# Performance work log

Measured on AMD Instinct MI355X. Metric: run time of the kernel, lower is better.

Reference implementation:

```python
import jax, jax.numpy as jnp
import numpy as np
from jax import lax

B, W_LEN, V, E, C, K, L = 8, 1000, 50000, 100, 50, 3, 18000


def setup_inputs() -> dict:
    key = jax.random.key(0)
    ks = jax.random.split(key, 7)
    return {
        "x": jax.random.randint(ks[0], (B, W_LEN), 0, V),
        "W_embed": jax.random.normal(ks[1], (V, E), dtype=jnp.float32) * 0.1,
        "conv_w": jax.random.normal(ks[2], (C, E, K), dtype=jnp.float32) * 0.08,
        "conv_b": jax.random.normal(ks[3], (C,), dtype=jnp.float32) * 0.01,
        "u_w": jax.random.normal(ks[4], (L, C), dtype=jnp.float32) * 0.1,
        "out_w": jax.random.normal(ks[5], (L, C), dtype=jnp.float32) * 0.1,
        "out_b": jax.random.normal(ks[6], (L,), dtype=jnp.float32) * 0.01,
    }


def reference(x, W_embed, conv_w, conv_b, u_w, out_w, out_b):
    # embedding lookup: (B, W, E)
    emb = W_embed[x]
    # conv1d over sequence, 'same' padding: (B, C, W)
    emb_ncw = jnp.transpose(emb, (0, 2, 1))
    H = lax.conv_general_dilated(
        emb_ncw, conv_w, window_strides=(1,), padding=[(K // 2, K // 2)],
        dimension_numbers=("NCH", "OIH", "NCH"))
    H = jnp.tanh(H + conv_b[None, :, None])
    H = jnp.transpose(H, (0, 2, 1))  # (B, W, C)
    # label-wise attention scores: (B, L, W), softmax over seq
    scores = jnp.einsum("lc,bwc->blw", u_w, H)
    attns = jax.nn.softmax(scores, axis=2)
    # attention-pooled reps: (B, L, C)
    m = jnp.einsum("blw,bwc->blc", attns, H)
    # per-label weighted dot product + bias, sigmoid: (B, L)
    out = jax.nn.sigmoid(jnp.sum(out_w[None] * m, axis=2) + out_b[None])
    return out
```

## Files before the change

kernel.cpp:

```cpp
#include <hip/hip_runtime.h>
#include <hip/hip_bf16.h>
#include <cmath>

#define AS1 __attribute__((address_space(1)))
#define AS3 __attribute__((address_space(3)))

#define B_ 8
#define W_LEN_ 1000
#define WP 1024
#define E_ 100
#define C_ 50
#define CPAD 64
#define HP 72
#define K_ 3
#define L_ 18000
#define TL 64
#define NLBLK ((L_ + TL - 1) / TL)
#define CWT 16
#define NSLOT (K_ * (E_ / 4))

typedef __attribute__((ext_vector_type(8))) short bf16x8;
typedef __attribute__((ext_vector_type(4))) short bf16x4;
typedef __attribute__((ext_vector_type(4))) float f32x4;

static __device__ __forceinline__ void gl_lds16(const void* g, void* l) {
    __builtin_amdgcn_global_load_lds((const AS1 unsigned*)g, (AS3 unsigned*)l, 16, 0, 0);
}
static __device__ __forceinline__ float bf2f(short s) {
    return __uint_as_float(((unsigned)(unsigned short)s) << 16);
}

__global__ __launch_bounds__(256) void prep_w(
    const float* __restrict__ conv_w, bf16x4* __restrict__ cwTs)
{
    int idx = blockIdx.x * blockDim.x + threadIdx.x;
    if (idx >= NSLOT * C_) return;
    int slot = idx / C_;
    int c    = idx % C_;
    int k = slot / (E_ / 4);
    int i = slot % (E_ / 4);
    bf16x4 v;
    #pragma unroll
    for (int q = 0; q < 4; q++) {
        __hip_bfloat16 h = __float2bfloat16(conv_w[((size_t)c * E_ + 4 * i + q) * K_ + k]);
        v[q] = *reinterpret_cast<short*>(&h);
    }
    cwTs[idx] = v;
}

__global__ __launch_bounds__(256) void prep_uo(
    const float* __restrict__ u_w, const float* __restrict__ out_w,
    __hip_bfloat16* __restrict__ UO)
{
    int tid = blockIdx.x * blockDim.x + threadIdx.x;
    if (tid >= 2 * L_ * CPAD) return;
    int c = tid & (CPAD - 1);
    int l = (tid >> 6) % L_;
    int m = tid / (L_ * CPAD);
    const float* src = m ? out_w : u_w;
    float v = (c < C_) ? src[(size_t)l * C_ + c] : 0.f;
    UO[tid] = __float2bfloat16(v);
}

__global__ __launch_bounds__(256) void conv_kernel(
    const int* __restrict__ x,
    const float* __restrict__ W_embed,
    const bf16x4* __restrict__ cwTs,
    const float* __restrict__ conv_b,
    __hip_bfloat16* __restrict__ H)
{
    __shared__ float4 emb_s[(CWT + 2) * (E_ / 4)];
    __shared__ bf16x4 wS[NSLOT * C_];

    const int b  = blockIdx.y;
    const int w0 = blockIdx.x * CWT;
    const int tid = threadIdx.x;

    for (int i = tid; i < NSLOT * C_; i += 256) wS[i] = cwTs[i];

    for (int i = tid; i < (CWT + 2) * (E_ / 4); i += 256) {
        int row = i / (E_ / 4);
        int e4  = i % (E_ / 4);
        int ws  = w0 - 1 + row;
        float4 v = make_float4(0.f, 0.f, 0.f, 0.f);
        if ((unsigned)ws < (unsigned)W_LEN_)
            v = ((const float4*)(W_embed + (size_t)x[b * W_LEN_ + ws] * E_))[e4];
        emb_s[i] = v;
    }
    __syncthreads();

    const int c  = tid & 63;
    const int wq = tid >> 6;
    const int cc = (c < C_) ? c : 0;

    f32x4 acc[4];
    const float bias = conv_b[cc];
    #pragma unroll
    for (int j = 0; j < 4; j++) acc[j] = (f32x4){bias, 0.f, 0.f, 0.f};

    const float4* eb = &emb_s[wq * 4 * (E_ / 4)];

    #pragma unroll 5
    for (int i = 0; i < E_ / 4; i++) {
        bf16x4 kb0 = wS[i * C_ + cc];
        bf16x4 kb1 = wS[(25 + i) * C_ + cc];
        bf16x4 kb2 = wS[(50 + i) * C_ + cc];
        float4 k0 = make_float4(bf2f(kb0[0]), bf2f(kb0[1]), bf2f(kb0[2]), bf2f(kb0[3]));
        float4 k1 = make_float4(bf2f(kb1[0]), bf2f(kb1[1]), bf2f(kb1[2]), bf2f(kb1[3]));
        float4 k2 = make_float4(bf2f(kb2[0]), bf2f(kb2[1]), bf2f(kb2[2]), bf2f(kb2[3]));
        float4 e0 = eb[i],       e1 = eb[25 + i],  e2 = eb[50 + i];
        float4 e3 = eb[75 + i],  e4 = eb[100 + i], e5 = eb[125 + i];
        acc[0].x += e0.x*k0.x + e1.x*k1.x + e2.x*k2.x;
        acc[0].y += e0.y*k0.y + e1.y*k1.y + e2.y*k2.y;
        acc[0].z += e0.z*k0.z + e1.z*k1.z + e2.z*k2.z;
        acc[0].w += e0.w*k0.w + e1.w*k1.w + e2.w*k2.w;
        acc[1].x += e1.x*k0.x + e2.x*k1.x + e3.x*k2.x;
        acc[1].y += e1.y*k0.y + e2.y*k1.y + e3.y*k2.y;
        acc[1].z += e1.z*k0.z + e2.z*k1.z + e3.z*k2.z;
        acc[1].w += e1.w*k0.w + e2.w*k1.w + e3.w*k2.w;
        acc[2].x += e2.x*k0.x + e3.x*k1.x + e4.x*k2.x;
        acc[2].y += e2.y*k0.y + e3.y*k1.y + e4.y*k2.y;
        acc[2].z += e2.z*k0.z + e3.z*k1.z + e4.z*k2.z;
        acc[2].w += e2.w*k0.w + e3.w*k1.w + e4.w*k2.w;
        acc[3].x += e3.x*k0.x + e4.x*k1.x + e5.x*k2.x;
        acc[3].y += e3.y*k0.y + e4.y*k1.y + e5.y*k2.y;
        acc[3].z += e3.z*k0.z + e4.z*k1.z + e5.z*k2.z;
        acc[3].w += e3.w*k0.w + e4.w*k1.w + e5.w*k2.w;
    }

    #pragma unroll
    for (int j = 0; j < 4; j++) {
        int w = w0 + wq * 4 + j;
        float v = 0.f;
        if (c < C_ && w < W_LEN_)
            v = tanhf((acc[j].x + acc[j].z) + (acc[j].y + acc[j].w));
        __hip_bfloat16* row = H + ((size_t)b * WP + w) * HP;
        row[c] = __float2bfloat16(v);
        if (c < HP - 64) row[64 + c] = __float2bfloat16(0.f);
    }
}

__global__ __launch_bounds__(256) void attn_kernel(
    const __hip_bfloat16* __restrict__ H,
    const __hip_bfloat16* __restrict__ UO,
    const float* __restrict__ out_b,
    float* __restrict__ out)
{
    __shared__ __hip_bfloat16 Hs[2][64 * HP];
    __shared__ float2 red[2][TL];

    const int b  = blockIdx.y;
    const int l0 = blockIdx.x * TL;
    const int tid  = threadIdx.x;
    const int lane = tid & 63;
    const int wid  = tid >> 6;
    const int mi = wid & 1, ni = wid >> 1;
    const int col = lane & 15, quad = lane >> 4;

    bf16x8 Uf[2][2], Of[2][2];
    #pragma unroll
    for (int mt = 0; mt < 2; mt++) {
        int l = l0 + mi * 32 + mt * 16 + col;
        if (l >= L_) l = L_ - 1;
        const __hip_bfloat16* up = UO + (size_t)l * CPAD + quad * 8;
        const __hip_bfloat16* op = up + (size_t)L_ * CPAD;
        #pragma unroll
        for (int st = 0; st < 2; st++) {
            Uf[mt][st] = *(const bf16x8*)(up + st * 32);
            Of[mt][st] = *(const bf16x8*)(op + st * 32);
        }
    }

    f32x4 lsum[2] = {{0.f,0.f,0.f,0.f},{0.f,0.f,0.f,0.f}};
    f32x4 num [2] = {{0.f,0.f,0.f,0.f},{0.f,0.f,0.f,0.f}};
    const f32x4 zero = {0.f, 0.f, 0.f, 0.f};

    const __hip_bfloat16* Hb = H + (size_t)b * WP * HP;

    {
        const char* g = (const char*)Hb;
        char* l = (char*)&Hs[0][0];
        gl_lds16(g + tid * 16,         l + tid * 16);
        gl_lds16(g + (tid + 256) * 16, l + (tid + 256) * 16);
        if (tid < 64)
            gl_lds16(g + (tid + 512) * 16, l + (tid + 512) * 16);
    }

    #pragma unroll 1
    for (int wt = 0; wt < WP; wt += 64) {
        const int cur = (wt >> 6) & 1;
        __syncthreads();

        if (wt + 64 < WP) {
            const char* g = (const char*)(Hb + (size_t)(wt + 64) * HP);
            char* l = (char*)&Hs[cur ^ 1][0];
            gl_lds16(g + tid * 16,         l + tid * 16);
            gl_lds16(g + (tid + 256) * 16, l + (tid + 256) * 16);
            if (tid < 64)
                gl_lds16(g + (tid + 512) * 16, l + (tid + 512) * 16);
        }

        bf16x8 Bc[2][2];
        #pragma unroll
        for (int nt = 0; nt < 2; nt++)
            #pragma unroll
            for (int st = 0; st < 2; st++)
                Bc[nt][st] = *(const bf16x8*)(&Hs[cur][(ni * 32 + nt * 16 + col) * HP
                                                       + quad * 8 + st * 32]);

        #pragma unroll
        for (int nt = 0; nt < 2; nt++) {
            #pragma unroll
            for (int mt = 0; mt < 2; mt++) {
                f32x4 S = __builtin_amdgcn_mfma_f32_16x16x32_bf16(Uf[mt][0], Bc[nt][0], zero, 0, 0, 0);
                S       = __builtin_amdgcn_mfma_f32_16x16x32_bf16(Uf[mt][1], Bc[nt][1], S,    0, 0, 0);
                f32x4 T = __builtin_amdgcn_mfma_f32_16x16x32_bf16(Of[mt][0], Bc[nt][0], zero, 0, 0, 0);
                T       = __builtin_amdgcn_mfma_f32_16x16x32_bf16(Of[mt][1], Bc[nt][1], T,    0, 0, 0);
                #pragma unroll
                for (int r = 0; r < 4; r++) {
                    float p = __expf(S[r]);
                    lsum[mt][r] += p;
                    num [mt][r] += p * T[r];
                }
            }
        }
    }

    #pragma unroll
    for (int mt = 0; mt < 2; mt++) {
        #pragma unroll
        for (int r = 0; r < 4; r++) {
            float ls = lsum[mt][r], nm = num[mt][r];
            #pragma unroll
            for (int d = 1; d < 16; d <<= 1) {
                ls += __shfl_xor(ls, d, 64);
                nm += __shfl_xor(nm, d, 64);
            }
            if (col == 0)
                red[ni][mi * 32 + mt * 16 + quad * 4 + r] = make_float2(ls, nm);
        }
    }
    __syncthreads();

    if (tid < TL) {
        int l = l0 + tid;
        if (l < L_) {
            float2 p0 = red[0][tid], p1 = red[1][tid];
            float z = (p0.y + p1.y) / (p0.x + p1.x - (float)(WP - W_LEN_)) + out_b[l];
            out[(size_t)b * L_ + l] = 1.f / (1.f + __expf(-z));
        }
    }
}

extern "C" void kernel_launch(void* const* d_in, const int* in_sizes, int n_in,
                              void* d_out, int out_size, void* d_ws, size_t ws_size,
                              hipStream_t stream) {
    const int*   x       = (const int*)  d_in[0];
    const float* W_embed = (const float*)d_in[1];
    const float* conv_w  = (const float*)d_in[2];
    const float* conv_b  = (const float*)d_in[3];
    const float* u_w     = (const float*)d_in[4];
    const float* out_w   = (const float*)d_in[5];
    const float* out_b   = (const float*)d_in[6];
    float* out = (float*)d_out;

    char* ws = (char*)d_ws;
    __hip_bfloat16* H  = (__hip_bfloat16*)ws;
    __hip_bfloat16* UO = (__hip_bfloat16*)(ws + 1179648);
    bf16x4*       cwTs = (bf16x4*)(ws + 1179648 + 4608000);

    {
        const int total = NSLOT * C_;
        prep_w<<<dim3((total + 255) / 256), 256, 0, stream>>>(conv_w, cwTs);
    }
    {
        const int total = 2 * L_ * CPAD;
        prep_uo<<<dim3((total + 255) / 256), 256, 0, stream>>>(u_w, out_w, UO);
    }
    {
        dim3 grid(WP / CWT, B_);
        conv_kernel<<<grid, 256, 0, stream>>>(x, W_embed, cwTs, conv_b, H);
    }
    {
        dim3 grid(NLBLK, B_);
        attn_kernel<<<grid, 256, 0, stream>>>(H, UO, out_b, out);
    }
}
```

Before: 153.4 us.

## Merge prep kernels, drop H padding, per-wave swizzled LDS pipeline in attention

Fuses the two weight-prep kernels into one launch that also vectorizes the UO conversion and pre-scales u_w by log2(e) so the softmax can use exp2. H rows shrink from 72 to 64 bf16 columns, and the attention kernel moves to 128 threads. Each wave now owns its own double-buffered LDS tile, loaded with an XOR-style swizzle to avoid bank conflicts, which removes the per-iteration __syncthreads. Each wave covers all 64 labels, which reuses each H fragment across more MFMAs but doubles the per-thread fragment and accumulator registers and halves the threads per block.

```diff
diff --git a/kernel.cpp b/kernel.cpp
--- a/kernel.cpp
+++ b/kernel.cpp
@@ -11,13 +11,13 @@
 #define E_ 100
 #define C_ 50
 #define CPAD 64
-#define HP 72
 #define K_ 3
 #define L_ 18000
 #define TL 64
 #define NLBLK ((L_ + TL - 1) / TL)
 #define CWT 16
 #define NSLOT (K_ * (E_ / 4))
+#define LOG2E 1.4426950408889634f
 
 typedef __attribute__((ext_vector_type(8))) short bf16x8;
 typedef __attribute__((ext_vector_type(4))) short bf16x4;
@@ -30,36 +30,42 @@
     return __uint_as_float(((unsigned)(unsigned short)s) << 16);
 }
 
-__global__ __launch_bounds__(256) void prep_w(
-    const float* __restrict__ conv_w, bf16x4* __restrict__ cwTs)
+__global__ __launch_bounds__(256) void prep_kernel(
+    const float* __restrict__ conv_w,
+    const float* __restrict__ u_w, const float* __restrict__ out_w,
+    bf16x4* __restrict__ cwTs, bf16x4* __restrict__ UO4)
 {
-    int idx = blockIdx.x * blockDim.x + threadIdx.x;
-    if (idx >= NSLOT * C_) return;
-    int slot = idx / C_;
-    int c    = idx % C_;
-    int k = slot / (E_ / 4);
-    int i = slot % (E_ / 4);
-    bf16x4 v;
-    #pragma unroll
-    for (int q = 0; q < 4; q++) {
-        __hip_bfloat16 h = __float2bfloat16(conv_w[((size_t)c * E_ + 4 * i + q) * K_ + k]);
-        v[q] = *reinterpret_cast<short*>(&h);
-    }
-    cwTs[idx] = v;
-}
-
-__global__ __launch_bounds__(256) void prep_uo(
-    const float* __restrict__ u_w, const float* __restrict__ out_w,
-    __hip_bfloat16* __restrict__ UO)
-{
-    int tid = blockIdx.x * blockDim.x + threadIdx.x;
-    if (tid >= 2 * L_ * CPAD) return;
-    int c = tid & (CPAD - 1);
-    int l = (tid >> 6) % L_;
-    int m = tid / (L_ * CPAD);
-    const float* src = m ? out_w : u_w;
-    float v = (c < C_) ? src[(size_t)l * C_ + c] : 0.f;
-    UO[tid] = __float2bfloat16(v);
+    if (blockIdx.x < 15) {
+        int idx = blockIdx.x * 256 + threadIdx.x;
+        if (idx >= NSLOT * C_) return;
+        int slot = idx / C_;
+        int c    = idx % C_;
+        int k = slot / (E_ / 4);
+        int i = slot % (E_ / 4);
+        bf16x4 v;
+        #pragma unroll
+        for (int q = 0; q < 4; q++) {
+            __hip_bfloat16 h = __float2bfloat16(conv_w[((size_t)c * E_ + 4 * i + q) * K_ + k]);
+            v[q] = *reinterpret_cast<short*>(&h);
+        }
+        cwTs[idx] = v;
+    } else {
+        int idx = (blockIdx.x - 15) * 256 + threadIdx.x;
+        if (idx >= 2 * L_ * (CPAD / 4)) return;
+        int c4 = idx & 15;
+        int l  = (idx >> 4) % L_;
+        int m  = idx / (L_ * 16);
+        const float* src = m ? out_w : u_w;
+        const float scale = m ? 1.f : LOG2E;
+        bf16x4 v;
+        #pragma unroll
+        for (int q = 0; q < 4; q++) {
+            int c = c4 * 4 + q;
+            __hip_bfloat16 h = __float2bfloat16(c < C_ ? src[(size_t)l * C_ + c] * scale : 0.f);
+            v[q] = *reinterpret_cast<short*>(&h);
+        }
+        UO4[idx] = v;
+    }
 }
 
 __global__ __launch_bounds__(256) void conv_kernel(
@@ -134,33 +140,30 @@
         float v = 0.f;
         if (c < C_ && w < W_LEN_)
             v = tanhf((acc[j].x + acc[j].z) + (acc[j].y + acc[j].w));
-        __hip_bfloat16* row = H + ((size_t)b * WP + w) * HP;
-        row[c] = __float2bfloat16(v);
-        if (c < HP - 64) row[64 + c] = __float2bfloat16(0.f);
-    }
-}
-
-__global__ __launch_bounds__(256) void attn_kernel(
+        H[((size_t)b * WP + w) * 64 + c] = __float2bfloat16(v);
+    }
+}
+
+__global__ __launch_bounds__(128) void attn_kernel(
     const __hip_bfloat16* __restrict__ H,
     const __hip_bfloat16* __restrict__ UO,
     const float* __restrict__ out_b,
     float* __restrict__ out)
 {
-    __shared__ __hip_bfloat16 Hs[2][64 * HP];
+    __shared__ __hip_bfloat16 Hs[2][2][32 * 64];
     __shared__ float2 red[2][TL];
 
     const int b  = blockIdx.y;
     const int l0 = blockIdx.x * TL;
     const int tid  = threadIdx.x;
     const int lane = tid & 63;
-    const int wid  = tid >> 6;
-    const int mi = wid & 1, ni = wid >> 1;
+    const int ni   = tid >> 6;
     const int col = lane & 15, quad = lane >> 4;
 
-    bf16x8 Uf[2][2], Of[2][2];
-    #pragma unroll
-    for (int mt = 0; mt < 2; mt++) {
-        int l = l0 + mi * 32 + mt * 16 + col;
+    bf16x8 Uf[4][2], Of[4][2];
+    #pragma unroll
+    for (int mt = 0; mt < 4; mt++) {
+        int l = l0 + mt * 16 + col;
         if (l >= L_) l = L_ - 1;
         const __hip_bfloat16* up = UO + (size_t)l * CPAD + quad * 8;
         const __hip_bfloat16* op = up + (size_t)L_ * CPAD;
@@ -171,63 +174,69 @@
         }
     }
 
-    f32x4 lsum[2] = {{0.f,0.f,0.f,0.f},{0.f,0.f,0.f,0.f}};
-    f32x4 num [2] = {{0.f,0.f,0.f,0.f},{0.f,0.f,0.f,0.f}};
+    f32x4 lsum[4], num[4];
+    #pragma unroll
+    for (int mt = 0; mt < 4; mt++) { lsum[mt] = (f32x4){0,0,0,0}; num[mt] = (f32x4){0,0,0,0}; }
     const f32x4 zero = {0.f, 0.f, 0.f, 0.f};
 
-    const __hip_bfloat16* Hb = H + (size_t)b * WP * HP;
-
-    {
-        const char* g = (const char*)Hb;
-        char* l = (char*)&Hs[0][0];
-        gl_lds16(g + tid * 16,         l + tid * 16);
-        gl_lds16(g + (tid + 256) * 16, l + (tid + 256) * 16);
-        if (tid < 64)
-            gl_lds16(g + (tid + 512) * 16, l + (tid + 512) * 16);
-    }
+    int goff[4];
+    #pragma unroll
+    for (int s = 0; s < 4; s++) {
+        int p  = s * 64 + lane;
+        int r  = p >> 3;
+        int pc = p & 7;
+        int q  = (pc - r) & 7;
+        goff[s] = (ni * 32 + r) * 64 + q * 8;
+    }
+
+    const __hip_bfloat16* Hb = H + (size_t)b * WP * 64;
+    char* lbase = (char*)&Hs[ni][0][0];
+
+    #pragma unroll
+    for (int s = 0; s < 4; s++)
+        gl_lds16((const char*)(Hb + goff[s]), lbase + s * 1024 + lane * 16);
 
     #pragma unroll 1
     for (int wt = 0; wt < WP; wt += 64) {
         const int cur = (wt >> 6) & 1;
-        __syncthreads();
 
         if (wt + 64 < WP) {
-            const char* g = (const char*)(Hb + (size_t)(wt + 64) * HP);
-            char* l = (char*)&Hs[cur ^ 1][0];
-            gl_lds16(g + tid * 16,         l + tid * 16);
-            gl_lds16(g + (tid + 256) * 16, l + (tid + 256) * 16);
-            if (tid < 64)
-                gl_lds16(g + (tid + 512) * 16, l + (tid + 512) * 16);
+            const __hip_bfloat16* g = Hb + (size_t)(wt + 64) * 64;
+            char* l = lbase + (cur ^ 1) * 4096;
+            #pragma unroll
+            for (int s = 0; s < 4; s++)
+                gl_lds16((const char*)(g + goff[s]), l + s * 1024 + lane * 16);
         }
 
         bf16x8 Bc[2][2];
         #pragma unroll
-        for (int nt = 0; nt < 2; nt++)
+        for (int nt = 0; nt < 2; nt++) {
+            int r = nt * 16 + col;
             #pragma unroll
             for (int st = 0; st < 2; st++)
-                Bc[nt][st] = *(const bf16x8*)(&Hs[cur][(ni * 32 + nt * 16 + col) * HP
-                                                       + quad * 8 + st * 32]);
+                Bc[nt][st] = *(const bf16x8*)(&Hs[ni][cur][r * 64 + ((quad + 4 * st + r) & 7) * 8]);
+        }
 
         #pragma unroll
         for (int nt = 0; nt < 2; nt++) {
             #pragma unroll
-            for (int mt = 0; mt < 2; mt++) {
+            for (int mt = 0; mt < 4; mt++) {
                 f32x4 S = __builtin_amdgcn_mfma_f32_16x16x32_bf16(Uf[mt][0], Bc[nt][0], zero, 0, 0, 0);
                 S       = __builtin_amdgcn_mfma_f32_16x16x32_bf16(Uf[mt][1], Bc[nt][1], S,    0, 0, 0);
                 f32x4 T = __builtin_amdgcn_mfma_f32_16x16x32_bf16(Of[mt][0], Bc[nt][0], zero, 0, 0, 0);
                 T       = __builtin_amdgcn_mfma_f32_16x16x32_bf16(Of[mt][1], Bc[nt][1], T,    0, 0, 0);
                 #pragma unroll
                 for (int r = 0; r < 4; r++) {
-                    float p = __expf(S[r]);
+                    float p = __builtin_amdgcn_exp2f(S[r]);
                     lsum[mt][r] += p;
-                    num [mt][r] += p * T[r];
+                    num [mt][r] = fmaf(p, T[r], num[mt][r]);
                 }
             }
         }
     }
 
     #pragma unroll
-    for (int mt = 0; mt < 2; mt++) {
+    for (int mt = 0; mt < 4; mt++) {
         #pragma unroll
         for (int r = 0; r < 4; r++) {
             float ls = lsum[mt][r], nm = num[mt][r];
@@ -237,7 +246,7 @@
                 nm += __shfl_xor(nm, d, 64);
             }
             if (col == 0)
-                red[ni][mi * 32 + mt * 16 + quad * 4 + r] = make_float2(ls, nm);
+                red[ni][mt * 16 + quad * 4 + r] = make_float2(ls, nm);
         }
     }
     __syncthreads();
@@ -266,16 +275,13 @@
 
     char* ws = (char*)d_ws;
     __hip_bfloat16* H  = (__hip_bfloat16*)ws;
-    __hip_bfloat16* UO = (__hip_bfloat16*)(ws + 1179648);
-    bf16x4*       cwTs = (bf16x4*)(ws + 1179648 + 4608000);
+    __hip_bfloat16* UO = (__hip_bfloat16*)(ws + 1048576);
+    bf16x4*       cwTs = (bf16x4*)(ws + 1048576 + 4608000);
 
     {
-        const int total = NSLOT * C_;
-        prep_w<<<dim3((total + 255) / 256), 256, 0, stream>>>(conv_w, cwTs);
-    }
-    {
-        const int total = 2 * L_ * CPAD;
-        prep_uo<<<dim3((total + 255) / 256), 256, 0, stream>>>(u_w, out_w, UO);
+        const int uo_blocks = (2 * L_ * (CPAD / 4) + 255) / 256;
+        prep_kernel<<<dim3(15 + uo_blocks), 256, 0, stream>>>(conv_w, u_w, out_w,
+                                                              cwTs, (bf16x4*)UO);
     }
     {
         dim3 grid(WP / CWT, B_);
@@ -283,6 +289,6 @@
     }
     {
         dim3 grid(NLBLK, B_);
-        attn_kernel<<<grid, 256, 0, stream>>>(H, UO, out_b, out);
-    }
-}
+        attn_kernel<<<grid, 128, 0, stream>>>(H, UO, out_b, out);
+    }
+}
```

New measurement: 153.6 us. Within noise of the previous version (+0.1%).
